# Performance work log

Hardware: AMD Instinct MI355X
Metric: run time of the kernel (lower is better)

## Reference

```python
import jax, jax.numpy as jnp
import numpy as np

ALPHA = 0.2  # LeakyReLU negative slope


def setup_inputs() -> dict:
    key = jax.random.key(0)
    k1, k2, k3, k4 = jax.random.split(key, 4)
    bs, n, fin = 8, 1024, 256
    heads, fo = 8, 64
    h = jax.random.normal(k1, (bs, n, fin), dtype=jnp.float32)
    adj = jax.random.randint(k2, (bs, n, n), 0, 2, dtype=jnp.int32)
    # W stored as [in_features, heads*out] so Wh = h @ W (same math as torch Linear)
    W = jax.random.normal(k3, (fin, heads * fo), dtype=jnp.float32) * 0.1
    a = jax.random.normal(k4, (heads, 2 * fo), dtype=jnp.float32) * 0.1
    return {"h": h, "adj": adj, "W": W, "a": a}


def reference(h, adj, W, a):
    bs, n, _ = h.shape
    heads, two_fo = a.shape
    fo = two_fo // 2
    # Wh: [bs, n, heads, fo]
    Wh = (h @ W).reshape(bs, n, heads, fo)
    a_src, a_dst = a[:, :fo], a[:, fo:]
    # Additive attention decomposed: e[b,h,i,j] = leaky_relu(src[b,h,i] + dst[b,h,j])
    e_src = jnp.einsum('bnhf,hf->bhn', Wh, a_src)  # [bs, heads, n]
    e_dst = jnp.einsum('bnhf,hf->bhn', Wh, a_dst)
    e = e_src[:, :, :, None] + e_dst[:, :, None, :]  # [bs, heads, n, n]
    e = jnp.where(e > 0, e, ALPHA * e)  # LeakyReLU
    e = jnp.where(adj[:, None, :, :] == 0, -jnp.inf, e)
    attn = jax.nn.softmax(e, axis=-1)  # [bs, heads, n, n]
    # h_prime[b,i,h,f] = sum_j attn[b,h,i,j] * Wh[b,j,h,f]
    h_prime = jnp.einsum('bhij,bjhf->bihf', attn, Wh)
    return h_prime.reshape(bs, n, heads * fo)
```

## Files before the change

### kernel.cpp

```cpp
#include <hip/hip_runtime.h>
#include <hip/hip_bf16.h>
#include <math.h>

#define BS 8
#define NN 1024
#define FIN 256
#define HEADS 8
#define FO 64
#define NH (HEADS*FO)
static constexpr float ALPHA = 0.2f;
static constexpr float LOG2E = 1.4426950408889634f;

typedef short bf16x8 __attribute__((ext_vector_type(8)));
typedef float f32x4  __attribute__((ext_vector_type(4)));
typedef float f32x2  __attribute__((ext_vector_type(2)));
typedef unsigned short u16;
typedef unsigned u32;
typedef u16 u16x4v __attribute__((ext_vector_type(4)));
typedef u16 u16x8v __attribute__((ext_vector_type(8)));

__device__ __forceinline__ u16 f2b(float x) {
    __hip_bfloat16 b = __float2bfloat16(x);
    return *reinterpret_cast<u16*>(&b);
}
__device__ __forceinline__ float fexp2(float x) {
#if __has_builtin(__builtin_amdgcn_exp2f)
    return __builtin_amdgcn_exp2f(x);
#else
    float r; asm("v_exp_f32 %0, %1" : "=v"(r) : "v"(x)); return r;
#endif
}
__device__ __forceinline__ void gload_lds16(const void* g, void* l) {
    __builtin_amdgcn_global_load_lds(
        (const __attribute__((address_space(1))) unsigned int*)g,
        (__attribute__((address_space(3))) unsigned int*)l, 16, 0, 0);
}

__global__ __launch_bounds__(256) void prep_misc(const float* __restrict__ h,
                                                 const int* __restrict__ adj,
                                                 const float* __restrict__ W,
                                                 u16* __restrict__ hb,
                                                 u16* __restrict__ WbT,
                                                 u32* __restrict__ bits) {
    const int bid = blockIdx.x;
    const int t = threadIdx.x;
    if (bid < 8192) {
        const int lane = t & 63;
        const size_t e0 = ((size_t)bid * 256 + t) * 4;
        const int4 v = *reinterpret_cast<const int4*>(adj + e0);
        u32 x = (v.x ? 1u : 0u) | (v.y ? 2u : 0u) | (v.z ? 4u : 0u) | (v.w ? 8u : 0u);
        {   const u32 r = (u32)__shfl_xor((int)x, 1);
            const int sh = (lane & 1) * 4;  x = (x << sh) | (r << (4 - sh)); }
        {   const u32 r = (u32)__shfl_xor((int)x, 2);
            const int sh = (lane & 2) * 4;  x = (x << sh) | (r << (8 - sh)); }
        {   const u32 r = (u32)__shfl_xor((int)x, 4);
            const int sh = (lane & 4) * 4;  x = (x << sh) | (r << (16 - sh)); }
        if ((lane & 7) == 0) bits[e0 >> 5] = x;
    } else if (bid < 9216) {
        const int i = ((bid - 8192) * 256 + t) * 8;
        const float4 v0 = *reinterpret_cast<const float4*>(h + i);
        const float4 v1 = *reinterpret_cast<const float4*>(h + i + 4);
        u16x8v o;
        o[0]=f2b(v0.x); o[1]=f2b(v0.y); o[2]=f2b(v0.z); o[3]=f2b(v0.w);
        o[4]=f2b(v1.x); o[5]=f2b(v1.y); o[6]=f2b(v1.z); o[7]=f2b(v1.w);
        *reinterpret_cast<u16x8v*>(hb + i) = o;
    } else {
        __shared__ float T[64][65];
        const int bb = bid - 9216;
        const int hh = bb & 7;
        const int n0 = hh * 64, k0 = (bb >> 3) * 64;
        const int r4 = t >> 6, c = t & 63;
        #pragma unroll
        for (int p = 0; p < 16; ++p) {
            const int r = p * 4 + r4;
            T[r][c] = W[(size_t)(k0 + r) * NH + n0 + c];
        }
        __syncthreads();
        #pragma unroll
        for (int p = 0; p < 16; ++p) {
            const int r = p * 4 + r4;
            WbT[(size_t)(n0 + r) * FIN + k0 + c] = f2b(T[c][r]);
        }
    }
}

__global__ __launch_bounds__(256) void gemm_whT(const u16* __restrict__ hb,
                                                const u16* __restrict__ WbT,
                                                const float* __restrict__ avec,
                                                u16* __restrict__ WhT,
                                                float* __restrict__ esrc,
                                                float* __restrict__ edst) {
    __shared__ u16 Al[2][64 * 64];
    __shared__ u16 Bl[2][64 * 64];
    const int t = threadIdx.x, wv = t >> 6, lane = t & 63;
    const int g = lane >> 4, l15 = lane & 15;
    const int lid = (blockIdx.x & 7) * 128 + (blockIdx.x >> 3);
    const int m0 = (lid >> 3) * 64;
    const int h  = lid & 7;
    const int lr = lane >> 3;
    const int sch = (lane & 7) ^ lr;
    const int bh = (m0 >> 10) * HEADS + h;

    f32x4 acc[4] = {};

    auto stageA = [&](int buf, int k0) {
        #pragma unroll
        for (int c = 0; c < 2; ++c) {
            const int rowb = wv * 16 + c * 8;
            gload_lds16(hb + (size_t)(m0 + rowb + lr) * FIN + k0 + sch * 8,
                        &Al[buf][rowb * 64]);
        }
    };
    auto stageB = [&](int buf, int k0) {
        #pragma unroll
        for (int c = 0; c < 2; ++c) {
            const int rowb = wv * 16 + c * 8;
            gload_lds16(WbT + (size_t)(h * 64 + rowb + lr) * FIN + k0 + sch * 8,
                        &Bl[buf][rowb * 64]);
        }
    };

    stageA(0, 0); stageB(0, 0);
    __syncthreads();
    for (int kt = 0; kt < 4; ++kt) {
        const int buf = kt & 1;
        if (kt < 3) { stageA(buf ^ 1, (kt + 1) * 64); stageB(buf ^ 1, (kt + 1) * 64); }
        #pragma unroll
        for (int ks = 0; ks < 2; ++ks) {
            const int ch = (ks * 4 + g) ^ (l15 & 7);
            const bf16x8 afr = *reinterpret_cast<const bf16x8*>(
                &Al[buf][(wv * 16 + l15) * 64 + ch * 8]);
            #pragma unroll
            for (int n = 0; n < 4; ++n) {
                const bf16x8 bfr = *reinterpret_cast<const bf16x8*>(
                    &Bl[buf][(n * 16 + l15) * 64 + ch * 8]);
                acc[n] = __builtin_amdgcn_mfma_f32_16x16x32_bf16(afr, bfr, acc[n], 0, 0, 0);
            }
        }
        __syncthreads();
    }

    {
        float as_[4], ad_[4];
        #pragma unroll
        for (int n = 0; n < 4; ++n) {
            as_[n] = avec[h * 128 + n * 16 + l15] * LOG2E;
            ad_[n] = avec[h * 128 + 64 + n * 16 + l15] * LOG2E;
        }
        #pragma unroll
        for (int r = 0; r < 4; ++r) {
            float ps = acc[0][r] * as_[0] + acc[1][r] * as_[1]
                     + acc[2][r] * as_[2] + acc[3][r] * as_[3];
            float pd = acc[0][r] * ad_[0] + acc[1][r] * ad_[1]
                     + acc[2][r] * ad_[2] + acc[3][r] * ad_[3];
            #pragma unroll
            for (int off = 1; off < 16; off <<= 1) {
                ps += __shfl_xor(ps, off);
                pd += __shfl_xor(pd, off);
            }
            if (l15 == 0) {
                const int i = (m0 + wv * 16 + g * 4 + r) & (NN - 1);
                esrc[(size_t)bh * NN + i] = ps;
                edst[(size_t)bh * NN + i] = pd;
            }
        }
    }

    u16* scr = &Al[0][0];
    #pragma unroll
    for (int n = 0; n < 4; ++n) {
        u16x4v pk;
        #pragma unroll
        for (int r = 0; r < 4; ++r) pk[r] = f2b(acc[n][r]);
        *reinterpret_cast<u16x4v*>(&scr[(n * 16 + l15) * 72 + wv * 16 + g * 4]) = pk;
    }
    __syncthreads();
    const int il0 = m0 & (NN - 1);
    const int f = t >> 2, q = t & 3;
    const u16x8v v0 = *reinterpret_cast<const u16x8v*>(&scr[f * 72 + q * 16]);
    const u16x8v v1 = *reinterpret_cast<const u16x8v*>(&scr[f * 72 + q * 16 + 8]);
    u16* dst = &WhT[((size_t)bh * 64 + f) * NN + il0 + q * 16];
    *reinterpret_cast<u16x8v*>(dst)     = v0;
    *reinterpret_cast<u16x8v*>(dst + 8) = v1;
}

__global__ __launch_bounds__(256, 2) void attn_pv(const u32* __restrict__ bits,
                                                  const u16* __restrict__ WhT,
                                                  const float* __restrict__ esrc,
                                                  const float* __restrict__ edst,
                                                  float* __restrict__ out) {
    __shared__ u16 Bs[2][64 * 64];
    const int t = threadIdx.x, wv = t >> 6, lane = t & 63;
    const int g = lane >> 4, l15 = lane & 15;
    const int lr = lane >> 3, sch = (lane & 7) ^ lr;

    const int lid = (blockIdx.x & 7) * 64 + (blockIdx.x >> 3);
    const int it = lid & 7, h = (lid >> 3) & 7, b = lid >> 6;
    const int i0 = it * 128;
    const int bh = b * HEADS + h;
    const int row0 = i0 + wv * 32 + l15;

    const float es0 = esrc[(size_t)bh * NN + row0];
    const float es1 = esrc[(size_t)bh * NN + row0 + 16];
    const f32x2 es0v = {es0, es0};
    const f32x2 es1v = {es1, es1};
    const u16*  whb = WhT + (size_t)bh * 64 * NN;
    const float* ed = edst + (size_t)bh * NN + 8 * g;
    const u32*  bitrow0 = bits + (size_t)(b * NN + row0) * 32;
    const u32*  bitrow1 = bitrow0 + 16 * 32;

    auto stage = [&](int buf, int j0) {
        #pragma unroll
        for (int c = 0; c < 2; ++c) {
            const int fb = wv * 16 + c * 8;
            gload_lds16(whb + (size_t)(fb + lr) * NN + j0 + sch * 8,
                        &Bs[buf][fb * 64]);
        }
    };

    stage(0, 0);
    float4 peA[2], peB[2];
    u32    pw0[2], pw1[2];
    #pragma unroll
    for (int s = 0; s < 2; ++s) {
        peA[s] = *(const float4*)(ed + s * 32);
        peB[s] = *(const float4*)(ed + s * 32 + 4);
        pw0[s] = bitrow0[s];
        pw1[s] = bitrow1[s];
    }
    __syncthreads();

    f32x4 acc0[4] = {}, acc1[4] = {};
    f32x4 dsum0 = {}, dsum1 = {};
    bf16x8 ones;
    #pragma unroll
    for (int q = 0; q < 8; ++q) ones[q] = (short)0x3F80;

    for (int tt = 0; tt < 16; ++tt) {
        const int buf = tt & 1;
        const bool more = (tt < 15);
        if (more) {
            stage(buf ^ 1, (tt + 1) * 64);
            asm volatile("" ::: "memory");
        }
        #pragma unroll
        for (int ks = 0; ks < 2; ++ks) {
            const int s = tt * 2 + ks;
            const float4 e0 = peA[ks], e1 = peB[ks];
            const u32 w0 = pw0[ks], w1 = pw1[ks];
            if (more) {
                peA[ks] = *(const float4*)(ed + (s + 2) * 32);
                peB[ks] = *(const float4*)(ed + (s + 2) * 32 + 4);
                pw0[ks] = bitrow0[s + 2];
                pw1[ks] = bitrow1[s + 2];
            }
            const int chb = ((ks * 4 + g) ^ (l15 & 7)) * 8;
            const bf16x8 v0 = *(const bf16x8*)(&Bs[buf][(0 * 16 + l15) * 64 + chb]);
            const bf16x8 v1 = *(const bf16x8*)(&Bs[buf][(1 * 16 + l15) * 64 + chb]);
            const bf16x8 v2 = *(const bf16x8*)(&Bs[buf][(2 * 16 + l15) * 64 + chb]);
            const bf16x8 v3 = *(const bf16x8*)(&Bs[buf][(3 * 16 + l15) * 64 + chb]);

            f32x2 ej2[4];
            ej2[0] = f32x2{e0.x, e0.y};
            ej2[1] = f32x2{e0.z, e0.w};
            ej2[2] = f32x2{e1.x, e1.y};
            ej2[3] = f32x2{e1.z, e1.w};
            const u32 by0 = (w0 >> (8 * g)) & 0xffu;
            const u32 by1 = (w1 >> (8 * g)) & 0xffu;

            union { u32 u[4]; bf16x8 v; } af0, af1;
            #pragma unroll
            for (int qp = 0; qp < 4; ++qp) {
                f32x2 s0 = es0v + ej2[qp];
                f32x2 s1 = es1v + ej2[qp];
                s0 = __builtin_elementwise_max(s0, s0 * ALPHA);
                s1 = __builtin_elementwise_max(s1, s1 * ALPHA);
                const float p0a = fexp2(((by0 >> (2*qp))     & 1u) ? s0[0] : -1e30f);
                const float p0b = fexp2(((by0 >> (2*qp + 1)) & 1u) ? s0[1] : -1e30f);
                const float p1a = fexp2(((by1 >> (2*qp))     & 1u) ? s1[0] : -1e30f);
                const float p1b = fexp2(((by1 >> (2*qp + 1)) & 1u) ? s1[1] : -1e30f);
                union { __hip_bfloat162 b2; u32 w; } c0, c1;
                c0.b2 = __float22bfloat162_rn(make_float2(p0a, p0b));
                c1.b2 = __float22bfloat162_rn(make_float2(p1a, p1b));
                af0.u[qp] = c0.w;
                af1.u[qp] = c1.w;
            }
            __builtin_amdgcn_s_setprio(1);
            acc0[0] = __builtin_amdgcn_mfma_f32_16x16x32_bf16(af0.v, v0, acc0[0], 0, 0, 0);
            acc1[0] = __builtin_amdgcn_mfma_f32_16x16x32_bf16(af1.v, v0, acc1[0], 0, 0, 0);
            acc0[1] = __builtin_amdgcn_mfma_f32_16x16x32_bf16(af0.v, v1, acc0[1], 0, 0, 0);
            acc1[1] = __builtin_amdgcn_mfma_f32_16x16x32_bf16(af1.v, v1, acc1[1], 0, 0, 0);
            acc0[2] = __builtin_amdgcn_mfma_f32_16x16x32_bf16(af0.v, v2, acc0[2], 0, 0, 0);
            acc1[2] = __builtin_amdgcn_mfma_f32_16x16x32_bf16(af1.v, v2, acc1[2], 0, 0, 0);
            acc0[3] = __builtin_amdgcn_mfma_f32_16x16x32_bf16(af0.v, v3, acc0[3], 0, 0, 0);
            acc1[3] = __builtin_amdgcn_mfma_f32_16x16x32_bf16(af1.v, v3, acc1[3], 0, 0, 0);
            dsum0   = __builtin_amdgcn_mfma_f32_16x16x32_bf16(af0.v, ones, dsum0, 0, 0, 0);
            dsum1   = __builtin_amdgcn_mfma_f32_16x16x32_bf16(af1.v, ones, dsum1, 0, 0, 0);
            __builtin_amdgcn_s_setprio(0);
        }
        if (more) {
            asm volatile("s_waitcnt vmcnt(8)" ::: "memory");
            __builtin_amdgcn_s_barrier();
        }
    }

    float inv0[4], inv1[4];
    #pragma unroll
    for (int r = 0; r < 4; ++r) { inv0[r] = 1.0f / dsum0[r]; inv1[r] = 1.0f / dsum1[r]; }
    #pragma unroll
    for (int n = 0; n < 4; ++n)
        #pragma unroll
        for (int r = 0; r < 4; ++r) {
            const int io0 = i0 + wv * 32 + g * 4 + r;
            out[(size_t)(b * NN + io0) * NH + h * 64 + n * 16 + l15] =
                acc0[n][r] * inv0[r];
            out[(size_t)(b * NN + io0 + 16) * NH + h * 64 + n * 16 + l15] =
                acc1[n][r] * inv1[r];
        }
}

extern "C" void kernel_launch(void* const* d_in, const int* in_sizes, int n_in,
                              void* d_out, int out_size, void* d_ws, size_t ws_size,
                              hipStream_t stream) {
    const float* h   = (const float*)d_in[0];
    const int*   adj = (const int*)  d_in[1];
    const float* W   = (const float*)d_in[2];
    const float* a   = (const float*)d_in[3];
    float* out = (float*)d_out;

    char* p = (char*)d_ws;
    u16*   hb   = (u16*)p;   p += (size_t)BS * NN * FIN * 2;
    u16*   WbT  = (u16*)p;   p += (size_t)NH * FIN * 2;
    u16*   WhT  = (u16*)p;   p += (size_t)BS * HEADS * FO * NN * 2;
    float* esrc = (float*)p; p += (size_t)BS * HEADS * NN * 4;
    float* edst = (float*)p; p += (size_t)BS * HEADS * NN * 4;
    u32*   bits = (u32*)p;

    prep_misc<<<9248, 256, 0, stream>>>(h, adj, W, hb, WbT, bits);
    gemm_whT <<<1024, 256, 0, stream>>>(hb, WbT, a, WhT, esrc, edst);
    attn_pv  <<<512, 256, 0, stream>>>(bits, WhT, esrc, edst, out);
}
```

Before: 50.29 us.

## Double the staged key tile to 128 columns per LDS buffer

The attention-PV kernel now stages 128 key columns of WhT per double-buffer step instead of 64, with a new XOR swizzle over 16 chunks per row. The loop runs 8 iterations of 4 k-substeps instead of 16 of 2, halving barrier count and enlarging each prefetch. The initial __syncthreads is replaced with a vmcnt wait plus barrier. LDS use doubles to 64KB per block, which may limit occupancy under the 2-blocks launch bound, and the vmcnt thresholds must match the new outstanding load counts.

Measured after the change: 51.50 us. 1.02x slower.

```diff
diff --git a/kernel.cpp b/kernel.cpp
--- a/kernel.cpp
+++ b/kernel.cpp
@@ -189,10 +189,9 @@
                                                   const float* __restrict__ esrc,
                                                   const float* __restrict__ edst,
                                                   float* __restrict__ out) {
-    __shared__ u16 Bs[2][64 * 64];
+    __shared__ u16 Bs[2][128 * 64];
     const int t = threadIdx.x, wv = t >> 6, lane = t & 63;
     const int g = lane >> 4, l15 = lane & 15;
-    const int lr = lane >> 3, sch = (lane & 7) ^ lr;
 
     const int lid = (blockIdx.x & 7) * 64 + (blockIdx.x >> 3);
     const int it = lid & 7, h = (lid >> 3) & 7, b = lid >> 6;
@@ -211,10 +210,12 @@
 
     auto stage = [&](int buf, int j0) {
         #pragma unroll
-        for (int c = 0; c < 2; ++c) {
-            const int fb = wv * 16 + c * 8;
-            gload_lds16(whb + (size_t)(fb + lr) * NN + j0 + sch * 8,
-                        &Bs[buf][fb * 64]);
+        for (int c = 0; c < 4; ++c) {
+            const int fb = wv * 16 + c * 4;
+            const int f  = fb + (lane >> 4);
+            const int jg = (lane & 15) ^ (f & 15);
+            gload_lds16(whb + (size_t)f * NN + j0 + jg * 8,
+                        &Bs[buf][fb * 128]);
         }
     };
 
@@ -228,7 +229,8 @@
         pw0[s] = bitrow0[s];
         pw1[s] = bitrow1[s];
     }
-    __syncthreads();
+    asm volatile("s_waitcnt vmcnt(8)" ::: "memory");
+    __builtin_amdgcn_s_barrier();
 
     f32x4 acc0[4] = {}, acc1[4] = {};
     f32x4 dsum0 = {}, dsum1 = {};
@@ -236,29 +238,31 @@
     #pragma unroll
     for (int q = 0; q < 8; ++q) ones[q] = (short)0x3F80;
 
-    for (int tt = 0; tt < 16; ++tt) {
+    for (int tt = 0; tt < 8; ++tt) {
         const int buf = tt & 1;
-        const bool more = (tt < 15);
+        const bool more = (tt < 7);
         if (more) {
-            stage(buf ^ 1, (tt + 1) * 64);
+            stage(buf ^ 1, (tt + 1) * 128);
             asm volatile("" ::: "memory");
         }
-        #pragma unroll
-        for (int ks = 0; ks < 2; ++ks) {
-            const int s = tt * 2 + ks;
-            const float4 e0 = peA[ks], e1 = peB[ks];
-            const u32 w0 = pw0[ks], w1 = pw1[ks];
-            if (more) {
-                peA[ks] = *(const float4*)(ed + (s + 2) * 32);
-                peB[ks] = *(const float4*)(ed + (s + 2) * 32 + 4);
-                pw0[ks] = bitrow0[s + 2];
-                pw1[ks] = bitrow1[s + 2];
-            }
-            const int chb = ((ks * 4 + g) ^ (l15 & 7)) * 8;
-            const bf16x8 v0 = *(const bf16x8*)(&Bs[buf][(0 * 16 + l15) * 64 + chb]);
-            const bf16x8 v1 = *(const bf16x8*)(&Bs[buf][(1 * 16 + l15) * 64 + chb]);
-            const bf16x8 v2 = *(const bf16x8*)(&Bs[buf][(2 * 16 + l15) * 64 + chb]);
-            const bf16x8 v3 = *(const bf16x8*)(&Bs[buf][(3 * 16 + l15) * 64 + chb]);
+        const char* bsb0 = (const char*)&Bs[buf][0] + l15 * 256;
+        #pragma unroll
+        for (int ks = 0; ks < 4; ++ks) {
+            const int s = tt * 4 + ks;
+            const int sl = ks & 1;
+            const float4 e0 = peA[sl], e1 = peB[sl];
+            const u32 w0 = pw0[sl], w1 = pw1[sl];
+            if (s < 30) {
+                peA[sl] = *(const float4*)(ed + (s + 2) * 32);
+                peB[sl] = *(const float4*)(ed + (s + 2) * 32 + 4);
+                pw0[sl] = bitrow0[s + 2];
+                pw1[sl] = bitrow1[s + 2];
+            }
+            const int chb = (((ks * 4 + g) ^ l15) << 4);
+            const bf16x8 v0 = *(const bf16x8*)(bsb0 + chb);
+            const bf16x8 v1 = *(const bf16x8*)(bsb0 + 4096 + chb);
+            const bf16x8 v2 = *(const bf16x8*)(bsb0 + 8192 + chb);
+            const bf16x8 v3 = *(const bf16x8*)(bsb0 + 12288 + chb);
 
             f32x2 ej2[4];
             ej2[0] = f32x2{e0.x, e0.y};
@@ -299,7 +303,7 @@
             __builtin_amdgcn_s_setprio(0);
         }
         if (more) {
-            asm volatile("s_waitcnt vmcnt(8)" ::: "memory");
+            asm volatile("s_waitcnt vmcnt(16)" ::: "memory");
             __builtin_amdgcn_s_barrier();
         }
     }
```
